# Optimization experiments

Hardware: AMD Instinct MI355X
Metric: run time of the kernel (lower is better)

The kernel has to match this reference:

```python
import jax, jax.numpy as jnp
import numpy as np

# ---- config (matches init_kwargs) ----
ORIGIN_OCC_SHAPE = (16, 200, 200)   # (D_oi, H_oi, W_oi)
INPUT_SIZE = (900, 1600)            # (ih, iw)
DOWN_SAMPLE = 8
GRID_CONFIG = {
    'x_bound': [-40.0, 40.0, 0.4],
    'y_bound': [-40.0, 40.0, 0.4],
    'z_bound': [-1.0, 5.4, 0.4],
    'd_bound': [2.0, 58.0, 1.0],
}


def setup_inputs() -> dict:
    key = jax.random.key(0)
    occ_feature = jax.random.normal(key, (1, 32, 16, 200, 200), dtype=jnp.float32)
    # realistic nuScenes-like intrinsics
    K = jnp.array([[[1266.4, 0.0, 816.3],
                    [0.0, 1266.4, 491.5],
                    [0.0, 0.0, 1.0]]], dtype=jnp.float32)
    # cam->ego: camera looks along ego +x; cam z -> ego x, cam x -> ego -y, cam y -> ego -z
    T = jnp.array([[[0.0, 0.0, 1.0, 1.5],
                    [-1.0, 0.0, 0.0, 0.0],
                    [0.0, -1.0, 0.0, 1.5],
                    [0.0, 0.0, 0.0, 1.0]]], dtype=jnp.float32)
    return {'occ_feature': occ_feature, 'K': K, 'T': T}


def get_sampling_points():
    ih, iw = INPUT_SIZE
    fh, fw = ih // DOWN_SAMPLE, iw // DOWN_SAMPLE
    d0, d1, dstep = GRID_CONFIG['d_bound']
    fd = int((d1 - d0) // dstep)
    x = jnp.linspace(0.0, iw - 1.0, fw)
    y = jnp.linspace(0.0, ih - 1.0, fh)
    d = jnp.linspace(d0, d1, fd)
    gd, gy, gx = jnp.meshgrid(d, y, x, indexing='ij')   # (fd, fh, fw)
    # homogeneous image points scaled by depth: [x*d, y*d, d, 1]
    pts = jnp.stack([gx * gd, gy * gd, gd, jnp.ones_like(gd)], axis=-1)
    return pts  # (fd, fh, fw, 4)


def grid_sample_3d(vol, grid):
    """Trilinear grid_sample, padding_mode='zeros', align_corners=True.
    vol: (B,C,D,H,W); grid: (B,Do,Ho,Wo,3) with (x,y,z) in [-1,1] -> (W,H,D)."""
    B, C, D, H, W = vol.shape
    gx, gy, gz = grid[..., 0], grid[..., 1], grid[..., 2]
    x = (gx + 1.0) * 0.5 * (W - 1)
    y = (gy + 1.0) * 0.5 * (H - 1)
    z = (gz + 1.0) * 0.5 * (D - 1)
    x0 = jnp.floor(x); y0 = jnp.floor(y); z0 = jnp.floor(z)
    tx = x - x0; ty = y - y0; tz = z - z0
    vol_flat = vol.reshape(B, C, D * H * W)

    def corner(zc, yc, xc, w):
        valid = (xc >= 0) & (xc <= W - 1) & (yc >= 0) & (yc <= H - 1) & (zc >= 0) & (zc <= D - 1)
        zi = jnp.clip(zc, 0, D - 1).astype(jnp.int32)
        yi = jnp.clip(yc, 0, H - 1).astype(jnp.int32)
        xi = jnp.clip(xc, 0, W - 1).astype(jnp.int32)
        idx = ((zi * H + yi) * W + xi).reshape(B, 1, -1)          # (B,1,M)
        g = jnp.take_along_axis(vol_flat, idx, axis=2)            # (B,C,M)
        wm = jnp.where(valid, w, 0.0).reshape(B, 1, -1)
        return g * wm

    out = (corner(z0, y0, x0, (1 - tz) * (1 - ty) * (1 - tx))
           + corner(z0, y0, x0 + 1, (1 - tz) * (1 - ty) * tx)
           + corner(z0, y0 + 1, x0, (1 - tz) * ty * (1 - tx))
           + corner(z0, y0 + 1, x0 + 1, (1 - tz) * ty * tx)
           + corner(z0 + 1, y0, x0, tz * (1 - ty) * (1 - tx))
           + corner(z0 + 1, y0, x0 + 1, tz * (1 - ty) * tx)
           + corner(z0 + 1, y0 + 1, x0, tz * ty * (1 - tx))
           + corner(z0 + 1, y0 + 1, x0 + 1, tz * ty * tx))
    Do, Ho, Wo = grid.shape[1:4]
    return out.reshape(B, C, Do, Ho, Wo)


def volume_transform(occ_feature, K, T):
    B, C, D_occ, H_occ, W_occ = occ_feature.shape
    D_oi, H_oi, W_oi = ORIGIN_OCC_SHAPE
    ratio = (W_oi / W_occ, H_oi / H_occ, D_oi / D_occ)
    xb, yb, zb = GRID_CONFIG['x_bound'], GRID_CONFIG['y_bound'], GRID_CONFIG['z_bound']

    # ego -> ego-feature-grid affine (4x4)
    e2f = jnp.eye(4, dtype=jnp.float32)
    e2f = e2f.at[0, 0].set(1.0 / xb[2] / ratio[0])
    e2f = e2f.at[1, 1].set(1.0 / yb[2] / ratio[1])
    e2f = e2f.at[2, 2].set(1.0 / zb[2] / ratio[2])
    e2f = e2f.at[0, 3].set(-xb[0] / xb[2] / ratio[0])
    e2f = e2f.at[1, 3].set(-yb[0] / yb[2] / ratio[1])
    e2f = e2f.at[2, 3].set(-zb[0] / zb[2] / ratio[2])

    # cam2img 4x4 with K in top-left, then invert (matches torch.inverse path)
    cam2img = jnp.tile(jnp.eye(4, dtype=K.dtype)[None], (B, 1, 1))
    cam2img = cam2img.at[:, :3, :3].set(K)
    img2cam = jnp.linalg.inv(cam2img)                  # (B,4,4)

    # fused projection matrix: ego2egofeat @ T @ img2cam
    M = jnp.einsum('ij,bjk,bkl->bil', e2f, T, img2cam)  # (B,4,4)

    pts = get_sampling_points()                         # (fd,fh,fw,4)
    feat_pts = jnp.einsum('bij,dhwj->bdhwi', M, pts)[..., :3]  # (B,fd,fh,fw,3)

    norm = jnp.array([W_occ - 1, H_occ - 1, D_occ - 1], dtype=jnp.float32)
    grid = feat_pts / norm * 2.0 - 1.0

    sampled = grid_sample_3d(occ_feature, grid)         # (B,C,fd,fh,fw)
    return jnp.sum(sampled, axis=2)                     # (B,C,fh,fw)


def reference(occ_feature, K, T):
    return volume_transform(occ_feature, K, T)
```

## Files before the change

kernel.cpp:

```cpp
#include <hip/hip_runtime.h>

#define FD 56
#define FH 112
#define FW 200
#define VD 16
#define VH 200
#define VW 200
#define NC 32
#define NPIX (FH * FW)
#define CSTRIDE (VD * VH * VW)

typedef float f2v __attribute__((ext_vector_type(2)));
typedef f2v uf2v __attribute__((aligned(4)));

__global__ __launch_bounds__(256)
void VolumeTransform_3667902071054_kernel(const float* __restrict__ vol,
                                          const float* __restrict__ Km,
                                          const float* __restrict__ Tm,
                                          float* __restrict__ out) {
    __shared__ float sM[12];
    if (threadIdx.x == 0) {
        float a = Km[0], b = Km[1], c = Km[2];
        float d = Km[3], e = Km[4], f = Km[5];
        float g = Km[6], h = Km[7], i = Km[8];
        float A00 = e * i - f * h, A01 = c * h - b * i, A02 = b * f - c * e;
        float A10 = f * g - d * i, A11 = a * i - c * g, A12 = c * d - a * f;
        float A20 = d * h - e * g, A21 = b * g - a * h, A22 = a * e - b * d;
        float det = a * A00 + b * A10 + c * A20;
        float r = 1.0f / det;
        float Ki[9] = {A00 * r, A01 * r, A02 * r,
                       A10 * r, A11 * r, A12 * r,
                       A20 * r, A21 * r, A22 * r};
        float R[4][4];
        for (int rr = 0; rr < 4; ++rr) {
            for (int cc = 0; cc < 3; ++cc)
                R[rr][cc] = Tm[rr * 4 + 0] * Ki[0 * 3 + cc]
                          + Tm[rr * 4 + 1] * Ki[1 * 3 + cc]
                          + Tm[rr * 4 + 2] * Ki[2 * 3 + cc];
            R[rr][3] = Tm[rr * 4 + 3];
        }
        const float s[3] = {2.5f, 2.5f, 2.5f};
        const float t[3] = {100.0f, 100.0f, 2.5f};
        for (int rr = 0; rr < 3; ++rr)
            for (int cc = 0; cc < 4; ++cc)
                sM[rr * 4 + cc] = s[rr] * R[rr][cc] + t[rr] * R[3][cc];
    }
    __syncthreads();

    const int cg   = blockIdx.x & 3;
    const int pg   = blockIdx.x >> 2;
    const int lane = threadIdx.x & 63;
    const int wv   = threadIdx.x >> 6;
    const int c0   = (cg * 4 + wv) * 2;
    const int p    = pg * 64 + lane;
    const int py   = p / FW;
    const int px   = p - py * FW;

    const float gx = (float)px * (1599.0f / 199.0f);
    const float gy = (float)py * (899.0f / 111.0f);

    const float m03 = sM[3], m13 = sM[7], m23 = sM[11];
    const float ax = sM[0] * gx + sM[1] * gy + sM[2];
    const float ay = sM[4] * gx + sM[5] * gy + sM[6];
    const float az = sM[8] * gx + sM[9] * gy + sM[10];

    const float* __restrict__ volc0 = vol + (size_t)c0 * CSTRIDE;
    const float* __restrict__ volc1 = volc0 + CSTRIDE;
    float acc0 = 0.0f, acc1 = 0.0f;

    for (int k = 0; k < FD; ++k) {
        const float gd = 2.0f + (float)k * (56.0f / 55.0f);
        const float fx = ax * gd + m03;
        const float fy = ay * gd + m13;
        const float fz = az * gd + m23;

        if (!(fx > -1.0f && fx < (float)VW &&
              fy > -1.0f && fy < (float)VH &&
              fz > -1.0f && fz < (float)VD))
            continue;

        const float xf = floorf(fx), yf = floorf(fy), zf = floorf(fz);
        const float tx = fx - xf, ty = fy - yf, tz = fz - zf;
        const int ix = (int)xf, iy = (int)yf, iz = (int)zf;

        const float wy0 = (iy >= 0)     ? (1.0f - ty) : 0.0f;
        const float wy1 = (iy < VH - 1) ? ty          : 0.0f;
        const float wz0 = (iz >= 0)     ? (1.0f - tz) : 0.0f;
        const float wz1 = (iz < VD - 1) ? tz          : 0.0f;

        const float w00 = wz0 * wy0, w01 = wz0 * wy1;
        const float w10 = wz1 * wy0, w11 = wz1 * wy1;

        const int yo0 = max(iy, 0) * VW;
        const int yo1 = min(iy + 1, VH - 1) * VW;
        const int zo0 = max(iz, 0) * (VH * VW);
        const int zo1 = min(iz + 1, VD - 1) * (VH * VW);

        float h00a, h01a, h10a, h11a;
        float h00b, h01b, h10b, h11b;

        if (ix >= 0 && ix < VW - 1) {
            const int o00 = zo0 + yo0 + ix, o01 = zo0 + yo1 + ix;
            const int o10 = zo1 + yo0 + ix, o11 = zo1 + yo1 + ix;
            const float wx0 = 1.0f - tx, wx1 = tx;
            f2v a00 = *(const uf2v*)(volc0 + o00);
            f2v a01 = *(const uf2v*)(volc0 + o01);
            f2v a10 = *(const uf2v*)(volc0 + o10);
            f2v a11 = *(const uf2v*)(volc0 + o11);
            f2v b00 = *(const uf2v*)(volc1 + o00);
            f2v b01 = *(const uf2v*)(volc1 + o01);
            f2v b10 = *(const uf2v*)(volc1 + o10);
            f2v b11 = *(const uf2v*)(volc1 + o11);
            h00a = wx0 * a00.x + wx1 * a00.y;  h01a = wx0 * a01.x + wx1 * a01.y;
            h10a = wx0 * a10.x + wx1 * a10.y;  h11a = wx0 * a11.x + wx1 * a11.y;
            h00b = wx0 * b00.x + wx1 * b00.y;  h01b = wx0 * b01.x + wx1 * b01.y;
            h10b = wx0 * b10.x + wx1 * b10.y;  h11b = wx0 * b11.x + wx1 * b11.y;
        } else {
            const float wx0 = (ix >= 0)     ? (1.0f - tx) : 0.0f;
            const float wx1 = (ix < VW - 1) ? tx          : 0.0f;
            const int xi0 = max(ix, 0);
            const int xi1 = min(ix + 1, VW - 1);
            h00a = wx0 * volc0[zo0 + yo0 + xi0] + wx1 * volc0[zo0 + yo0 + xi1];
            h01a = wx0 * volc0[zo0 + yo1 + xi0] + wx1 * volc0[zo0 + yo1 + xi1];
            h10a = wx0 * volc0[zo1 + yo0 + xi0] + wx1 * volc0[zo1 + yo0 + xi1];
            h11a = wx0 * volc0[zo1 + yo1 + xi0] + wx1 * volc0[zo1 + yo1 + xi1];
            h00b = wx0 * volc1[zo0 + yo0 + xi0] + wx1 * volc1[zo0 + yo0 + xi1];
            h01b = wx0 * volc1[zo0 + yo1 + xi0] + wx1 * volc1[zo0 + yo1 + xi1];
            h10b = wx0 * volc1[zo1 + yo0 + xi0] + wx1 * volc1[zo1 + yo0 + xi1];
            h11b = wx0 * volc1[zo1 + yo1 + xi0] + wx1 * volc1[zo1 + yo1 + xi1];
        }

        acc0 += w00 * h00a + w01 * h01a + w10 * h10a + w11 * h11a;
        acc1 += w00 * h00b + w01 * h01b + w10 * h10b + w11 * h11b;
    }

    out[c0 * NPIX + p]       = acc0;
    out[(c0 + 1) * NPIX + p] = acc1;
}

extern "C" void kernel_launch(void* const* d_in, const int* in_sizes, int n_in,
                              void* d_out, int out_size, void* d_ws, size_t ws_size,
                              hipStream_t stream) {
    (void)in_sizes; (void)n_in; (void)out_size; (void)d_ws; (void)ws_size;
    const float* vol = (const float*)d_in[0];
    const float* Km  = (const float*)d_in[1];
    const float* Tm  = (const float*)d_in[2];
    float* out = (float*)d_out;

    VolumeTransform_3667902071054_kernel<<<dim3(1400), dim3(256), 0, stream>>>(vol, Km, Tm, out);
}
```

Measured before the change: 165.6 us.

## Clip depth loop to analytic valid range and make sampling branchless

Each pixel now solves for the depth interval where its projected ray lies inside the volume and iterates only over that range of depth samples, with a one-sample margin, instead of testing all 56. Inside the loop the per-sample bounds `continue` and the separate edge path for x are replaced by masked weights and a single clamped float2-load path, and the loop is unrolled by 2. This aims to cut wasted iterations and wave divergence. In exchange, every iteration in the range now issues its loads even when the sample is masked out.

```diff
diff --git a/kernel.cpp b/kernel.cpp
--- a/kernel.cpp
+++ b/kernel.cpp
@@ -64,71 +64,81 @@
     const float ay = sM[4] * gx + sM[5] * gy + sM[6];
     const float az = sM[8] * gx + sM[9] * gy + sM[10];
 
+    float dlo = 2.0f, dhi = 58.0f;
+    {
+        const float A[3]  = {ax, ay, az};
+        const float Bv[3] = {m03, m13, m23};
+        const float HI[3] = {(float)VW, (float)VH, (float)VD};
+        for (int q = 0; q < 3; ++q) {
+            float a = A[q], b = Bv[q], hi = HI[q];
+            if (a > 0.0f)      { dlo = fmaxf(dlo, (-1.0f - b) / a); dhi = fminf(dhi, (hi - b) / a); }
+            else if (a < 0.0f) { dlo = fmaxf(dlo, (hi - b) / a);    dhi = fminf(dhi, (-1.0f - b) / a); }
+            else if (!(b > -1.0f && b < hi)) { dlo = 1e30f; dhi = -1e30f; }
+        }
+    }
+    int klo = (int)ceilf((dlo - 2.0f) * (55.0f / 56.0f));
+    int khi = (int)floorf((dhi - 2.0f) * (55.0f / 56.0f));
+    klo = max(klo - 1, 0);
+    khi = min(khi + 1, FD - 1);
+
     const float* __restrict__ volc0 = vol + (size_t)c0 * CSTRIDE;
     const float* __restrict__ volc1 = volc0 + CSTRIDE;
     float acc0 = 0.0f, acc1 = 0.0f;
 
-    for (int k = 0; k < FD; ++k) {
+#pragma unroll 2
+    for (int k = klo; k <= khi; ++k) {
         const float gd = 2.0f + (float)k * (56.0f / 55.0f);
-        const float fx = ax * gd + m03;
-        const float fy = ay * gd + m13;
-        const float fz = az * gd + m23;
+        const float fx = fmaf(ax, gd, m03);
+        const float fy = fmaf(ay, gd, m13);
+        const float fz = fmaf(az, gd, m23);
 
-        if (!(fx > -1.0f && fx < (float)VW &&
-              fy > -1.0f && fy < (float)VH &&
-              fz > -1.0f && fz < (float)VD))
-            continue;
+        const bool valid = (fx > -1.0f) && (fx < (float)VW) &&
+                           (fy > -1.0f) && (fy < (float)VH) &&
+                           (fz > -1.0f) && (fz < (float)VD);
+        const float vm = valid ? 1.0f : 0.0f;
 
         const float xf = floorf(fx), yf = floorf(fy), zf = floorf(fz);
         const float tx = fx - xf, ty = fy - yf, tz = fz - zf;
         const int ix = (int)xf, iy = (int)yf, iz = (int)zf;
 
+        float wlo = (ix >= 0) ? (1.0f - tx) : tx;
+        wlo = (ix >= VW - 1) ? 0.0f : wlo;
+        float whi = (ix >= 0) ? tx : 0.0f;
+        whi = (ix >= VW - 1) ? (1.0f - tx) : whi;
+
         const float wy0 = (iy >= 0)     ? (1.0f - ty) : 0.0f;
         const float wy1 = (iy < VH - 1) ? ty          : 0.0f;
-        const float wz0 = (iz >= 0)     ? (1.0f - tz) : 0.0f;
-        const float wz1 = (iz < VD - 1) ? tz          : 0.0f;
-
+        const float wz0 = ((iz >= 0)     ? (1.0f - tz) : 0.0f) * vm;
+        const float wz1 = ((iz < VD - 1) ? tz          : 0.0f) * vm;
         const float w00 = wz0 * wy0, w01 = wz0 * wy1;
         const float w10 = wz1 * wy0, w11 = wz1 * wy1;
 
-        const int yo0 = max(iy, 0) * VW;
-        const int yo1 = min(iy + 1, VH - 1) * VW;
-        const int zo0 = max(iz, 0) * (VH * VW);
-        const int zo1 = min(iz + 1, VD - 1) * (VH * VW);
+        const int xi0 = min(max(ix, 0), VW - 2);
+        const int yo0 = min(max(iy,     0), VH - 1) * VW;
+        const int yo1 = min(max(iy + 1, 0), VH - 1) * VW;
+        const int zo0 = min(max(iz,     0), VD - 1) * (VH * VW);
+        const int zo1 = min(max(iz + 1, 0), VD - 1) * (VH * VW);
 
-        float h00a, h01a, h10a, h11a;
-        float h00b, h01b, h10b, h11b;
+        const int o00 = zo0 + yo0 + xi0, o01 = zo0 + yo1 + xi0;
+        const int o10 = zo1 + yo0 + xi0, o11 = zo1 + yo1 + xi0;
 
-        if (ix >= 0 && ix < VW - 1) {
-            const int o00 = zo0 + yo0 + ix, o01 = zo0 + yo1 + ix;
-            const int o10 = zo1 + yo0 + ix, o11 = zo1 + yo1 + ix;
-            const float wx0 = 1.0f - tx, wx1 = tx;
-            f2v a00 = *(const uf2v*)(volc0 + o00);
-            f2v a01 = *(const uf2v*)(volc0 + o01);
-            f2v a10 = *(const uf2v*)(volc0 + o10);
-            f2v a11 = *(const uf2v*)(volc0 + o11);
-            f2v b00 = *(const uf2v*)(volc1 + o00);
-            f2v b01 = *(const uf2v*)(volc1 + o01);
-            f2v b10 = *(const uf2v*)(volc1 + o10);
-            f2v b11 = *(const uf2v*)(volc1 + o11);
-            h00a = wx0 * a00.x + wx1 * a00.y;  h01a = wx0 * a01.x + wx1 * a01.y;
-            h10a = wx0 * a10.x + wx1 * a10.y;  h11a = wx0 * a11.x + wx1 * a11.y;
-            h00b = wx0 * b00.x + wx1 * b00.y;  h01b = wx0 * b01.x + wx1 * b01.y;
-            h10b = wx0 * b10.x + wx1 * b10.y;  h11b = wx0 * b11.x + wx1 * b11.y;
-        } else {
-            const float wx0 = (ix >= 0)     ? (1.0f - tx) : 0.0f;
-            const float wx1 = (ix < VW - 1) ? tx          : 0.0f;
-            const int xi0 = max(ix, 0);
-            const int xi1 = min(ix + 1, VW - 1);
-            h00a = wx0 * volc0[zo0 + yo0 + xi0] + wx1 * volc0[zo0 + yo0 + xi1];
-            h01a = wx0 * volc0[zo0 + yo1 + xi0] + wx1 * volc0[zo0 + yo1 + xi1];
-            h10a = wx0 * volc0[zo1 + yo0 + xi0] + wx1 * volc0[zo1 + yo0 + xi1];
-            h11a = wx0 * volc0[zo1 + yo1 + xi0] + wx1 * volc0[zo1 + yo1 + xi1];
-            h00b = wx0 * volc1[zo0 + yo0 + xi0] + wx1 * volc1[zo0 + yo0 + xi1];
-            h01b = wx0 * volc1[zo0 + yo1 + xi0] + wx1 * volc1[zo0 + yo1 + xi1];
-            h10b = wx0 * volc1[zo1 + yo0 + xi0] + wx1 * volc1[zo1 + yo0 + xi1];
-            h11b = wx0 * volc1[zo1 + yo1 + xi0] + wx1 * volc1[zo1 + yo1 + xi1];
-        }
+        const f2v a00 = *(const uf2v*)(volc0 + o00);
+        const f2v a01 = *(const uf2v*)(volc0 + o01);
+        const f2v a10 = *(const uf2v*)(volc0 + o10);
+        const f2v a11 = *(const uf2v*)(volc0 + o11);
+        const f2v b00 = *(const uf2v*)(volc1 + o00);
+        const f2v b01 = *(const uf2v*)(volc1 + o01);
+        const f2v b10 = *(const uf2v*)(volc1 + o10);
+        const f2v b11 = *(const uf2v*)(volc1 + o11);
+
+        const float h00a = wlo * a00.x + whi * a00.y;
+        const float h01a = wlo * a01.x + whi * a01.y;
+        const float h10a = wlo * a10.x + whi * a10.y;
+        const float h11a = wlo * a11.x + whi * a11.y;
+        const float h00b = wlo * b00.x + whi * b00.y;
+        const float h01b = wlo * b01.x + whi * b01.y;
+        const float h10b = wlo * b10.x + whi * b10.y;
+        const float h11b = wlo * b11.x + whi * b11.y;
 
         acc0 += w00 * h00a + w01 * h01a + w10 * h10a + w11 * h11a;
         acc1 += w00 * h00b + w01 * h01b + w10 * h10b + w11 * h11b;
```

New measurement: 168.7 us. No clear change (+1.8%).
